# Kernel tuning notes

Measured on AMD Instinct MI355X. Metric: run time of the kernel, lower is better.

Reference implementation:

```python
import jax, jax.numpy as jnp
import numpy as np

K_HEADS = 8
SMALL_VALUE = -32767.0  # -2**15 + 1.0


def setup_inputs() -> dict:
    key = jax.random.key(0)
    ks = jax.random.split(key, 12)
    B, Cx, Ct, N, T = 16, 256, 256, 170, 64
    c_in, c_out = Cx + Ct, 512
    s_in = 1.0 / np.sqrt(c_in)
    s_out = 1.0 / np.sqrt(c_out)
    return {
        "x": jax.random.normal(ks[0], (B, Cx, N, T), jnp.float32),
        "tem_embedding": jax.random.normal(ks[1], (B, Ct, N, T), jnp.float32),
        "Wq": jax.random.normal(ks[2], (c_out, c_in), jnp.float32) * s_in,
        "bq": jax.random.normal(ks[3], (c_out,), jnp.float32) * 0.01,
        "Wk": jax.random.normal(ks[4], (c_out, c_in), jnp.float32) * s_in,
        "bk": jax.random.normal(ks[5], (c_out,), jnp.float32) * 0.01,
        "Wv": jax.random.normal(ks[6], (c_out, c_in), jnp.float32) * s_in,
        "bv": jax.random.normal(ks[7], (c_out,), jnp.float32) * 0.01,
        "Wo": jax.random.normal(ks[8], (c_out, c_out), jnp.float32) * s_out,
        "bo": jax.random.normal(ks[9], (c_out,), jnp.float32) * 0.01,
    }


def reference(x, tem_embedding, Wq, bq, Wk, bk, Wv, bv, Wo, bo):
    T = x.shape[3]
    # concat temporal embedding (sliced to last T steps) on channel dim
    xin = jnp.concatenate([x, tem_embedding[:, :, :, -T:]], axis=1)  # [B, c_in, N, T]

    def conv1x1(W, b):
        return jnp.einsum('oc,bcnt->bont', W, xin) + b[None, :, None, None]

    q = conv1x1(Wq, bq)  # [B, c_out, N, T]
    k = conv1x1(Wk, bk)
    v = conv1x1(Wv, bv)

    B, C, N, _ = q.shape
    d = C // K_HEADS

    def heads(t):
        # torch.cat(torch.split(t, d, dim=1), dim=0): head-major batch stacking
        return jnp.transpose(t.reshape(B, K_HEADS, d, N, T), (1, 0, 3, 4, 2))  # [K,B,N,T,d]

    qh, kh, vh = heads(q), heads(k), heads(v)

    scores = jnp.einsum('kbntd,kbnsd->kbnts', qh, kh) / jnp.sqrt(jnp.float32(d))
    causal = jnp.tril(jnp.ones((T, T), dtype=bool))  # [T, T]
    scores = jnp.where(causal[None, None, None], scores, SMALL_VALUE)
    attn = jax.nn.softmax(scores, axis=-1)
    out = jnp.einsum('kbnts,kbnsd->kbntd', attn, vh)  # [K,B,N,T,d]

    # merge heads back to channel dim (head-major channel order)
    out = jnp.transpose(out, (1, 0, 4, 2, 3)).reshape(B, C, N, T)  # [B, c_out, N, T]
    y = jnp.einsum('oc,bcnt->bont', Wo, out) + bo[None, :, None, None]
    return jax.nn.relu(y)
```

## Files before the change

### kernel.cpp

```cpp
#include <hip/hip_runtime.h>
#include <cstdint>
#include <cstddef>

#define B_    16
#define N_    170
#define T_    64
#define NT_   (N_ * T_)
#define C_    512
#define KH_   8

typedef unsigned short u16;
typedef float  f32x4  __attribute__((ext_vector_type(4)));
typedef short  bf16x8 __attribute__((ext_vector_type(8)));

__device__ __forceinline__ u16 f2bf(float f) {
  union { float f; unsigned u; } v; v.f = f;
  unsigned r = v.u + 0x7fffu + ((v.u >> 16) & 1u);
  return (u16)(r >> 16);
}

#define GLDS16(g, l) \
  __builtin_amdgcn_global_load_lds((const __attribute__((address_space(1))) void*)(g), \
                                   (__attribute__((address_space(3))) void*)(l), 16, 0, 0)

__device__ __forceinline__ int xcd_swz(int orig, int n) {
  int q = n >> 3, r = n & 7;
  int xcd = orig & 7, idx = orig >> 3;
  return (xcd < r ? xcd * (q + 1) : r * (q + 1) + (xcd - r) * q) + idx;
}

__global__ __launch_bounds__(256) void wconv(const float* __restrict__ wq, const float* __restrict__ wk,
                                             const float* __restrict__ wv, const float* __restrict__ wo,
                                             const float* __restrict__ bq, const float* __restrict__ bk,
                                             const float* __restrict__ bv,
                                             u16* __restrict__ oq, u16* __restrict__ ok,
                                             u16* __restrict__ ov, u16* __restrict__ oo,
                                             float* __restrict__ obias) {
  int idx = blockIdx.x * 256 + threadIdx.x;
  int mat = idx >> 16;
  int off = (idx & 65535) * 4;
  const float* s = (mat == 0) ? wq : (mat == 1) ? wk : (mat == 2) ? wv : wo;
  u16* d = (mat == 0) ? oq : (mat == 1) ? ok : (mat == 2) ? ov : oo;
  float4 v = *(const float4*)(s + off);
  u16 o[4] = { f2bf(v.x), f2bf(v.y), f2bf(v.z), f2bf(v.w) };
  *(uint2*)(d + off) = *(uint2*)o;
  if (idx < 1536)
    obias[idx] = (idx < 512) ? bq[idx] : (idx < 1024) ? bk[idx - 512] : bv[idx - 1024];
}

__global__ __launch_bounds__(256) void concat_tr(const float* __restrict__ x,
                                                 const float* __restrict__ tem,
                                                 u16* __restrict__ xin_tm) {
  __shared__ u16 tile[64 * 72];
  int mt = blockIdx.x, ct = blockIdx.y, b = blockIdx.z;
  const float* src = (ct < 4) ? (x   + ((size_t)b * 256 + (size_t)ct * 64) * NT_)
                              : (tem + ((size_t)b * 256 + (size_t)(ct - 4) * 64) * NT_);
  int m0 = mt * 64;
  int tid = threadIdx.x;
  for (int g = tid; g < 1024; g += 256) {
    int row = g >> 4, part = (g & 15) * 4;
    float4 v = *(const float4*)(src + (size_t)row * NT_ + m0 + part);
    u16* t = &tile[row * 72 + part];
    t[0] = f2bf(v.x); t[1] = f2bf(v.y); t[2] = f2bf(v.z); t[3] = f2bf(v.w);
  }
  __syncthreads();
  for (int h = tid; h < 512; h += 256) {
    int mm = h >> 3, part = (h & 7) * 8;
    u16 vals[8];
#pragma unroll
    for (int e = 0; e < 8; e++) vals[e] = tile[(part + e) * 72 + mm];
    *(uint4*)(xin_tm + ((size_t)(b * NT_ + m0 + mm)) * 512 + ct * 64 + part) = *(uint4*)vals;
  }
}

template <int MODE>
__global__ __launch_bounds__(256) void gemm_bt(
    const u16* __restrict__ A, int lda, size_t aBatch,
    const u16* __restrict__ Bm, int ldb, size_t bBatch,
    void* __restrict__ Cv, int ldc, size_t cBatch, size_t matStride,
    const float* __restrict__ bias, int K) {
  constexpr int NBLK  = (MODE == 0) ? 1020 : 340;
  constexpr int NFAST = (MODE == 0) ? 12 : 4;
  __shared__ u16 As[128 * 32];
  __shared__ u16 Bs[128 * 32];
  __shared__ u16 cst[(MODE == 0) ? 128 * 136 : 16];

  int b = blockIdx.z;
  int lin = xcd_swz(blockIdx.x, NBLK);
  int fast = lin % NFAST, slow = lin / NFAST;
  int bxT = (MODE == 0) ? fast : slow;
  int ayT = (MODE == 0) ? slow : fast;
  int rowA0 = ayT * 128, rowB0 = bxT * 128;

  const u16* Ab = A + (size_t)b * aBatch;
  const u16* Bb = Bm + (size_t)b * bBatch;
  int tid = threadIdx.x;
  int lane = tid & 63, w = tid >> 6;
  int quad = lane >> 4, l15 = lane & 15;
  int wr = (w >> 1) * 64, wc = (w & 1) * 64;

  f32x4 acc[4][4];
#pragma unroll
  for (int i = 0; i < 4; i++)
#pragma unroll
    for (int j = 0; j < 4; j++) acc[i][j] = (f32x4){0.f, 0.f, 0.f, 0.f};

  for (int k0 = 0; k0 < K; k0 += 32) {
#pragma unroll
    for (int r = 0; r < 2; r++) {
      int chunk = tid + r * 256;
      int row = chunk >> 2, kk = (chunk & 3) * 8;
      const u16* ga = Ab + (size_t)(rowA0 + row) * lda + k0 + kk;
      GLDS16(ga, &As[(r * 256 + w * 64) * 8]);
      const u16* gb = Bb + (size_t)(rowB0 + row) * ldb + k0 + kk;
      GLDS16(gb, &Bs[(r * 256 + w * 64) * 8]);
    }
    __syncthreads();
    bf16x8 af[4], bfr[4];
#pragma unroll
    for (int i = 0; i < 4; i++) af[i]  = *(const bf16x8*)&As[(wr + i * 16 + l15) * 32 + quad * 8];
#pragma unroll
    for (int j = 0; j < 4; j++) bfr[j] = *(const bf16x8*)&Bs[(wc + j * 16 + l15) * 32 + quad * 8];
#pragma unroll
    for (int i = 0; i < 4; i++)
#pragma unroll
      for (int j = 0; j < 4; j++)
        acc[i][j] = __builtin_amdgcn_mfma_f32_16x16x32_bf16(af[i], bfr[j], acc[i][j], 0, 0, 0);
    __syncthreads();
  }

  int gr0 = rowA0 + wr, gc0 = rowB0 + wc;
  if constexpr (MODE == 0) {
    int mat  = bxT >> 2;
    int colb = (bxT & 3) * 128;
#pragma unroll
    for (int j = 0; j < 4; j++) {
      int lc = wc + j * 16 + l15;
      float bj = bias[rowB0 + lc];
#pragma unroll
      for (int i = 0; i < 4; i++) {
        int lr = wr + i * 16 + quad * 4;
#pragma unroll
        for (int r = 0; r < 4; r++)
          cst[(lr + r) * 136 + lc] = f2bf(acc[i][j][r] + bj);
      }
    }
    __syncthreads();
    u16* C = (u16*)Cv + (size_t)b * cBatch + (size_t)mat * matStride
           + (size_t)rowA0 * ldc + colb;
#pragma unroll
    for (int it = 0; it < 8; it++) {
      int chunk = tid + it * 256;
      int row = chunk >> 4, cc = (chunk & 15) * 8;
      *(uint4*)(C + (size_t)row * ldc + cc) = *(const uint4*)&cst[row * 136 + cc];
    }
  } else {
    float* C = (float*)Cv + (size_t)b * cBatch;
#pragma unroll
    for (int i = 0; i < 4; i++)
#pragma unroll
      for (int r = 0; r < 4; r++) {
        int R = gr0 + i * 16 + quad * 4 + r;
        float br = bias[R];
#pragma unroll
        for (int j = 0; j < 4; j++) {
          float v = acc[i][j][r] + br;
          C[(size_t)R * ldc + gc0 + j * 16 + l15] = fmaxf(v, 0.f);
        }
      }
  }
}

__global__ __launch_bounds__(256) void attn(const u16* __restrict__ q_tm,
                                            const u16* __restrict__ k_tm,
                                            const u16* __restrict__ v_tm,
                                            u16* __restrict__ ao_tm) {
  __shared__ u16 qsh[64 * 72], ksh[64 * 72], psh[64 * 72];
  __shared__ u16 vsh[64 * 66];
  int n = blockIdx.x, kh = blockIdx.y, b = blockIdx.z;
  int tid = threadIdx.x, lane = tid & 63, w = tid >> 6;
  int quad = lane >> 4, l15 = lane & 15;

  const u16* qbase = q_tm + ((size_t)(b * NT_ + n * 64)) * 512 + kh * 64;
  const u16* kbase = k_tm + ((size_t)(b * NT_ + n * 64)) * 512 + kh * 64;
  const u16* vbase = v_tm + ((size_t)(b * NT_ + n * 64)) * 512 + kh * 64;

  for (int g = tid; g < 512; g += 256) {
    int row = g >> 3, part = (g & 7) * 8;
    *(uint4*)&qsh[row * 72 + part] = *(const uint4*)(qbase + (size_t)row * 512 + part);
    *(uint4*)&ksh[row * 72 + part] = *(const uint4*)(kbase + (size_t)row * 512 + part);
    u16 tv[8];
    *(uint4*)tv = *(const uint4*)(vbase + (size_t)row * 512 + part);
#pragma unroll
    for (int e = 0; e < 8; e++) vsh[(part + e) * 66 + row] = tv[e];
  }
  __syncthreads();

  f32x4 sacc[4];
#pragma unroll
  for (int j = 0; j < 4; j++) sacc[j] = (f32x4){0.f, 0.f, 0.f, 0.f};
  bf16x8 aq[2];
#pragma unroll
  for (int kc = 0; kc < 2; kc++)
    aq[kc] = *(const bf16x8*)&qsh[(w * 16 + l15) * 72 + kc * 32 + quad * 8];
#pragma unroll
  for (int j = 0; j < 4; j++)
#pragma unroll
    for (int kc = 0; kc < 2; kc++) {
      bf16x8 bk = *(const bf16x8*)&ksh[(j * 16 + l15) * 72 + kc * 32 + quad * 8];
      sacc[j] = __builtin_amdgcn_mfma_f32_16x16x32_bf16(aq[kc], bk, sacc[j], 0, 0, 0);
    }

  float pv[4][4];
#pragma unroll
  for (int r = 0; r < 4; r++) {
    int t = w * 16 + quad * 4 + r;
    float m = -3.4e38f;
#pragma unroll
    for (int j = 0; j < 4; j++) {
      int s = j * 16 + l15;
      float v = sacc[j][r] * 0.125f;
      if (s > t) v = -32767.0f;
      pv[j][r] = v;
      m = fmaxf(m, v);
    }
#pragma unroll
    for (int off = 1; off < 16; off <<= 1) m = fmaxf(m, __shfl_xor(m, off, 16));
    float sum = 0.f;
#pragma unroll
    for (int j = 0; j < 4; j++) {
      float e = __expf(pv[j][r] - m);
      pv[j][r] = e;
      sum += e;
    }
#pragma unroll
    for (int off = 1; off < 16; off <<= 1) sum += __shfl_xor(sum, off, 16);
    float inv = 1.f / sum;
#pragma unroll
    for (int j = 0; j < 4; j++)
      psh[(size_t)t * 72 + j * 16 + l15] = f2bf(pv[j][r] * inv);
  }
  f32x4 oacc[4];
#pragma unroll
  for (int j = 0; j < 4; j++) oacc[j] = (f32x4){0.f, 0.f, 0.f, 0.f};
  bf16x8 ap[2];
#pragma unroll
  for (int kc = 0; kc < 2; kc++)
    ap[kc] = *(const bf16x8*)&psh[(w * 16 + l15) * 72 + kc * 32 + quad * 8];
#pragma unroll
  for (int dj = 0; dj < 4; dj++)
#pragma unroll
    for (int kc = 0; kc < 2; kc++) {
      bf16x8 bv;
      {
        const unsigned* vp = (const unsigned*)&vsh[(dj * 16 + l15) * 66 + kc * 32 + quad * 8];
        unsigned* bp = (unsigned*)&bv;
        bp[0] = vp[0]; bp[1] = vp[1]; bp[2] = vp[2]; bp[3] = vp[3];
      }
      oacc[dj] = __builtin_amdgcn_mfma_f32_16x16x32_bf16(ap[kc], bv, oacc[dj], 0, 0, 0);
    }

  u16* ob = ao_tm + ((size_t)(b * NT_ + n * 64)) * 512 + kh * 64;
#pragma unroll
  for (int dj = 0; dj < 4; dj++)
#pragma unroll
    for (int r = 0; r < 4; r++) {
      int t = w * 16 + quad * 4 + r, d = dj * 16 + l15;
      ob[(size_t)t * 512 + d] = f2bf(oacc[dj][r]);
    }
}

extern "C" void kernel_launch(void* const* d_in, const int* in_sizes, int n_in,
                              void* d_out, int out_size, void* d_ws, size_t ws_size,
                              hipStream_t stream) {
  const float* x   = (const float*)d_in[0];
  const float* tem = (const float*)d_in[1];
  const float* Wq  = (const float*)d_in[2];
  const float* bq  = (const float*)d_in[3];
  const float* Wk  = (const float*)d_in[4];
  const float* bk  = (const float*)d_in[5];
  const float* Wv  = (const float*)d_in[6];
  const float* bv  = (const float*)d_in[7];
  const float* Wo  = (const float*)d_in[8];
  const float* bo  = (const float*)d_in[9];
  float* out = (float*)d_out;

  const size_t E = (size_t)B_ * 512 * NT_;
  u16* xin_tm = (u16*)d_ws;
  u16* q_tm   = xin_tm + E;
  u16* k_tm   = q_tm + E;
  u16* v_tm   = k_tm + E;
  u16* wqkv   = v_tm + E;
  u16* wob    = wqkv + 786432;
  float* bqkv = (float*)(wob + 262144);
  u16* ao_tm  = xin_tm;

  const size_t sBNT = (size_t)NT_ * 512;

  wconv<<<1024, 256, 0, stream>>>(Wq, Wk, Wv, Wo, bq, bk, bv,
                                  wqkv, wqkv + 262144, wqkv + 524288, wob, bqkv);
  concat_tr<<<dim3(N_, 8, B_), 256, 0, stream>>>(x, tem, xin_tm);

  gemm_bt<0><<<dim3(1020, 1, B_), 256, 0, stream>>>(xin_tm, 512, sBNT,
                                                    wqkv, 512, (size_t)0,
                                                    q_tm, 512, sBNT, E, bqkv, 512);

  attn<<<dim3(N_, KH_, B_), 256, 0, stream>>>(q_tm, k_tm, v_tm, ao_tm);

  gemm_bt<2><<<dim3(340, 1, B_), 256, 0, stream>>>(wob, 512, (size_t)0,
                                                   ao_tm, 512, sBNT,
                                                   out, NT_, (size_t)512 * NT_, 0, bo, 512);
}
```

Measured before the change: 1.328 ms.

## Load GEMM MFMA fragments directly from global memory, drop LDS staging

The GEMM kernel no longer stages A/B tiles through shared memory with global_load_lds and barriers. Each wave now loads its bf16 fragments straight from global memory, with a fully unrolled K loop hard-coded to 512 and an occupancy hint of 3 blocks per SM. This removes the barriers and LDS round trips. In exchange, fragment reuse across waves now depends on the L1/L2 caches, and K is fixed at 512, ignoring the runtime argument.

```diff
diff --git a/kernel.cpp b/kernel.cpp
--- a/kernel.cpp
+++ b/kernel.cpp
@@ -18,10 +18,6 @@
   unsigned r = v.u + 0x7fffu + ((v.u >> 16) & 1u);
   return (u16)(r >> 16);
 }
-
-#define GLDS16(g, l) \
-  __builtin_amdgcn_global_load_lds((const __attribute__((address_space(1))) void*)(g), \
-                                   (__attribute__((address_space(3))) void*)(l), 16, 0, 0)
 
 __device__ __forceinline__ int xcd_swz(int orig, int n) {
   int q = n >> 3, r = n & 7;
@@ -74,16 +70,16 @@
 }
 
 template <int MODE>
-__global__ __launch_bounds__(256) void gemm_bt(
+__global__ __launch_bounds__(256, 3) void gemm_bt(
     const u16* __restrict__ A, int lda, size_t aBatch,
     const u16* __restrict__ Bm, int ldb, size_t bBatch,
     void* __restrict__ Cv, int ldc, size_t cBatch, size_t matStride,
     const float* __restrict__ bias, int K) {
+  (void)K;
+  constexpr int KK    = 512;
   constexpr int NBLK  = (MODE == 0) ? 1020 : 340;
   constexpr int NFAST = (MODE == 0) ? 12 : 4;
-  __shared__ u16 As[128 * 32];
-  __shared__ u16 Bs[128 * 32];
-  __shared__ u16 cst[(MODE == 0) ? 128 * 136 : 16];
+  __shared__ u16 cst[(MODE == 0) ? 17408 : 16];
 
   int b = blockIdx.z;
   int lin = xcd_swz(blockIdx.x, NBLK);
@@ -99,34 +95,33 @@
   int quad = lane >> 4, l15 = lane & 15;
   int wr = (w >> 1) * 64, wc = (w & 1) * 64;
 
+  const u16* ap[4];
+  const u16* bp[4];
+#pragma unroll
+  for (int i = 0; i < 4; i++)
+    ap[i] = Ab + (size_t)(rowA0 + wr + i * 16 + l15) * lda + quad * 8;
+#pragma unroll
+  for (int j = 0; j < 4; j++)
+    bp[j] = Bb + (size_t)(rowB0 + wc + j * 16 + l15) * ldb + quad * 8;
+
   f32x4 acc[4][4];
 #pragma unroll
   for (int i = 0; i < 4; i++)
 #pragma unroll
     for (int j = 0; j < 4; j++) acc[i][j] = (f32x4){0.f, 0.f, 0.f, 0.f};
 
-  for (int k0 = 0; k0 < K; k0 += 32) {
-#pragma unroll
-    for (int r = 0; r < 2; r++) {
-      int chunk = tid + r * 256;
-      int row = chunk >> 2, kk = (chunk & 3) * 8;
-      const u16* ga = Ab + (size_t)(rowA0 + row) * lda + k0 + kk;
-      GLDS16(ga, &As[(r * 256 + w * 64) * 8]);
-      const u16* gb = Bb + (size_t)(rowB0 + row) * ldb + k0 + kk;
-      GLDS16(gb, &Bs[(r * 256 + w * 64) * 8]);
-    }
-    __syncthreads();
+#pragma unroll
+  for (int t = 0; t < KK / 32; t++) {
     bf16x8 af[4], bfr[4];
 #pragma unroll
-    for (int i = 0; i < 4; i++) af[i]  = *(const bf16x8*)&As[(wr + i * 16 + l15) * 32 + quad * 8];
-#pragma unroll
-    for (int j = 0; j < 4; j++) bfr[j] = *(const bf16x8*)&Bs[(wc + j * 16 + l15) * 32 + quad * 8];
+    for (int i = 0; i < 4; i++) af[i]  = *(const bf16x8*)(ap[i] + t * 32);
+#pragma unroll
+    for (int j = 0; j < 4; j++) bfr[j] = *(const bf16x8*)(bp[j] + t * 32);
 #pragma unroll
     for (int i = 0; i < 4; i++)
 #pragma unroll
       for (int j = 0; j < 4; j++)
         acc[i][j] = __builtin_amdgcn_mfma_f32_16x16x32_bf16(af[i], bfr[j], acc[i][j], 0, 0, 0);
-    __syncthreads();
   }
 
   int gr0 = rowA0 + wr, gc0 = rowB0 + wc;
```

New measurement: 1.989 ms. +49.8%, slower.
